# Kernel tuning notes

Hardware: AMD Instinct MI355X
Metric: run time of the kernel (lower is better)

The kernel has to match this reference:

```python
import jax, jax.numpy as jnp
import numpy as np

D_MODEL = 1024
NUM_HEAD = 16
D_K = D_MODEL // NUM_HEAD


def setup_inputs() -> dict:
    key = jax.random.key(0)
    ks = jax.random.split(key, 11)
    B, S = 2, 2048
    s = 1.0 / np.sqrt(D_MODEL)
    return {
        "q": jax.random.normal(ks[0], (B, S, D_MODEL), jnp.float32),
        "k": jax.random.normal(ks[1], (B, S, D_MODEL), jnp.float32),
        "v": jax.random.normal(ks[2], (B, S, D_MODEL), jnp.float32),
        "Wq": jax.random.normal(ks[3], (D_MODEL, D_MODEL), jnp.float32) * s,
        "bq": jnp.zeros((D_MODEL,), jnp.float32),
        "Wk": jax.random.normal(ks[4], (D_MODEL, D_MODEL), jnp.float32) * s,
        "bk": jnp.zeros((D_MODEL,), jnp.float32),
        "Wv": jax.random.normal(ks[5], (D_MODEL, D_MODEL), jnp.float32) * s,
        "bv": jnp.zeros((D_MODEL,), jnp.float32),
        "Wo": jax.random.normal(ks[6], (D_MODEL, D_MODEL), jnp.float32) * s,
        "bo": jnp.zeros((D_MODEL,), jnp.float32),
    }


def _split_head(x, B):
    # [B, S, d_model] -> [B, H, S, d_k]
    S = x.shape[1]
    return x.reshape(B, S, NUM_HEAD, D_K).transpose(0, 2, 1, 3)


def reference(q, k, v, Wq, bq, Wk, bk, Wv, bv, Wo, bo):
    B = q.shape[0]
    qh = _split_head(q @ Wq + bq, B)  # [B,H,Sq,dk]
    kh = _split_head(k @ Wk + bk, B)  # [B,H,Sk,dk]
    vh = _split_head(v @ Wv + bv, B)  # [B,H,Sk,dk]
    scores = jnp.einsum("bhqd,bhkd->bhqk", qh, kh) / jnp.sqrt(
        jnp.asarray(D_K, qh.dtype)
    )
    attn = jax.nn.softmax(scores, axis=-1)
    out = jnp.einsum("bhqk,bhkd->bhqd", attn, vh)  # [B,H,Sq,dk]
    out = out.transpose(0, 2, 1, 3).reshape(B, -1, D_MODEL)
    return jax.nn.relu(out @ Wo + bo)
```

## Files before the change

kernel.cpp:

```cpp
#include <hip/hip_runtime.h>
#include <math.h>

#define SEQ 2048
#define NHD 16

typedef float f32x4 __attribute__((ext_vector_type(4), may_alias));
typedef _Float16 h16x8 __attribute__((ext_vector_type(8), may_alias));
typedef _Float16 h16x4 __attribute__((ext_vector_type(4), may_alias));

__device__ __forceinline__ void gl_lds16(const void* g, void* l) {
  __builtin_amdgcn_global_load_lds(
      (const __attribute__((address_space(1))) unsigned int*)g,
      (__attribute__((address_space(3))) unsigned int*)l, 16, 0, 0);
}

struct PrepArgs {
  const float* W[4];
  _Float16* T[4];
  const float* X[3];
  _Float16* H[3];
};

__global__ __launch_bounds__(256) void prep_k(PrepArgs a) {
  __shared__ float tile[64][65];
  const int blk = blockIdx.x;
  const int t = threadIdx.x;
  if (blk < 1024) {
    const int widx = blk >> 8, tl = blk & 255;
    const int nb = (tl & 15) * 64, kb = (tl >> 4) * 64;
    const float* __restrict__ W = a.W[widx];
    _Float16* __restrict__ T = a.T[widx];
    const int c = t & 63, r0 = t >> 6;
#pragma unroll
    for (int i = 0; i < 16; ++i) {
      const int r = i * 4 + r0;
      tile[r][c] = W[(size_t)(kb + r) * 1024 + nb + c];
    }
    __syncthreads();
#pragma unroll
    for (int i = 0; i < 16; ++i) {
      const int n = i * 4 + r0;
      T[(size_t)(nb + n) * 1024 + kb + c] = (_Float16)tile[c][n];
    }
  } else {
    const int b2 = blk - 1024;
    const int z = b2 >> 11, bx = b2 & 2047;
    const float* __restrict__ X = a.X[z];
    _Float16* __restrict__ H = a.H[z];
    const size_t i = ((size_t)bx * 256 + t) * 8;
    const f32x4 f0 = *(const f32x4*)(X + i);
    const f32x4 f1 = *(const f32x4*)(X + i + 4);
    const float fs[8] = {f0.x, f0.y, f0.z, f0.w, f1.x, f1.y, f1.z, f1.w};
    h16x8 o;
#pragma unroll
    for (int j = 0; j < 8; ++j) o[j] = (_Float16)fs[j];
    *(h16x8*)(H + i) = o;
  }
}

struct QKVArgs {
  const _Float16* A[3];
  const _Float16* Bt[3];
  const float* bias[3];
  _Float16* C[3];
};

__global__ __launch_bounds__(512, 2) void gemm_qkv_k(QKVArgs a) {
  __shared__ __align__(16) char smem[131072];
  const int dblk = blockIdx.x;
  const int z = dblk >> 6;
  const int rb = dblk & 63;
  const int m0 = (rb >> 2) * 256;
  const int n0 = (rb & 3) * 256;
  const _Float16* __restrict__ A = a.A[z];
  const _Float16* __restrict__ Bt = a.Bt[z];
  const float* __restrict__ bias = a.bias[z];
  _Float16* __restrict__ C = a.C[z];

  const int t = threadIdx.x;
  const int l = t & 63, w = t >> 6;
  const int quad = l >> 4, l15 = l & 15;
  const int wm = w >> 2, wn = w & 3;

  const int srow = t >> 3;
  const int sslot = (t & 7) ^ (srow & 7);
  size_t goffA[4], goffB[4];
#pragma unroll
  for (int j = 0; j < 4; ++j) {
    goffA[j] = (size_t)(m0 + j * 64 + srow) * 1024 + sslot * 8;
    goffB[j] = (size_t)(n0 + j * 64 + srow) * 1024 + sslot * 8;
  }

  auto stage = [&](int buf, int kt) {
    const int k0 = kt * 64;
    char* base = smem + buf * 65536;
#pragma unroll
    for (int j = 0; j < 4; ++j) {
      gl_lds16(A + goffA[j] + k0, base + j * 8192 + w * 1024);
      gl_lds16(Bt + goffB[j] + k0, base + 32768 + j * 8192 + w * 1024);
    }
  };

  const f32x4 z4 = {0.f, 0.f, 0.f, 0.f};
  f32x4 acc[8][4];
#pragma unroll
  for (int i = 0; i < 8; ++i)
#pragma unroll
    for (int j = 0; j < 4; ++j) acc[i][j] = z4;

  const int xr = l15 & 7;

  stage(0, 0);
  for (int kt = 0; kt < 16; ++kt) {
    const int cur = kt & 1;
    if (kt < 15) {
      stage(cur ^ 1, kt + 1);
      asm volatile("s_waitcnt vmcnt(8)" ::: "memory");
    } else {
      asm volatile("s_waitcnt vmcnt(0)" ::: "memory");
    }
    __builtin_amdgcn_sched_barrier(0);
    __builtin_amdgcn_s_barrier();

    const char* base = smem + cur * 65536;
    h16x8 bf[4][2];
#pragma unroll
    for (int nj = 0; nj < 4; ++nj) {
      const int rowB = wn * 64 + nj * 16 + l15;
#pragma unroll
      for (int h = 0; h < 2; ++h) {
        const int sl = (h * 4 + quad) ^ xr;
        bf[nj][h] = *(const h16x8*)(base + 32768 + rowB * 128 + sl * 16);
      }
    }
#pragma unroll
    for (int mi = 0; mi < 8; ++mi) {
      const int rowA = wm * 128 + mi * 16 + l15;
      const h16x8 af0 = *(const h16x8*)(base + rowA * 128 + ((quad ^ xr) * 16));
      const h16x8 af1 = *(const h16x8*)(base + rowA * 128 + (((4 + quad) ^ xr) * 16));
#pragma unroll
      for (int nj = 0; nj < 4; ++nj) {
        acc[mi][nj] = __builtin_amdgcn_mfma_f32_16x16x32_f16(af0, bf[nj][0], acc[mi][nj], 0, 0, 0);
        acc[mi][nj] = __builtin_amdgcn_mfma_f32_16x16x32_f16(af1, bf[nj][1], acc[mi][nj], 0, 0, 0);
      }
    }
    __builtin_amdgcn_sched_barrier(0);
    __builtin_amdgcn_s_barrier();
  }

  if (z < 2) {
#pragma unroll
    for (int mi = 0; mi < 8; ++mi)
#pragma unroll
      for (int nj = 0; nj < 4; ++nj) {
        const int col = n0 + wn * 64 + nj * 16 + l15;
        const float bv = bias[col];
#pragma unroll
        for (int r = 0; r < 4; ++r) {
          const int row = m0 + wm * 128 + mi * 16 + quad * 4 + r;
          const int b = row >> 11, s = row & 2047;
          const int h = col >> 6, d = col & 63;
          C[((size_t)(b * NHD + h) * SEQ + s) * 64 + d] = (_Float16)(acc[mi][nj][r] + bv);
        }
      }
  } else {
    _Float16* sh = (_Float16*)smem;
#pragma unroll
    for (int mi = 0; mi < 8; ++mi)
#pragma unroll
      for (int nj = 0; nj < 4; ++nj) {
        const int col = wn * 64 + nj * 16 + l15;
        const float bv = bias[n0 + col];
#pragma unroll
        for (int r = 0; r < 4; ++r) {
          const int row = wm * 128 + mi * 16 + quad * 4 + r;
          sh[row * 256 + col] = (_Float16)(acc[mi][nj][r] + bv);
        }
      }
    __syncthreads();
    const int dr = t >> 1;
    const int half = t & 1;
    const int hh = dr >> 6, d = dr & 63;
    const int b = m0 >> 11, sbase = m0 & 2047;
    const int colL = hh * 64 + d;
    const size_t gbase =
        ((size_t)((b * NHD + (n0 >> 6) + hh) * 64 + d)) * SEQ + sbase + half * 128;
#pragma unroll
    for (int m8 = 0; m8 < 16; ++m8) {
      const int qq = half * 128 + m8 * 8;
      h16x8 ov;
#pragma unroll
      for (int j = 0; j < 8; ++j) {
        const int q = qq + j;
        const int g = q >> 6, p = q & 63;
        const int c = (((p >> 5) << 1) | ((p >> 2) & 1)) * 16 +
                      (((p >> 3) & 3) << 2) + (p & 3);
        ov[j] = sh[(g * 64 + c) * 256 + colL];
      }
      *(h16x8*)(C + gbase + m8 * 8) = ov;
    }
  }
}

__global__ __launch_bounds__(256) void gemm_o_k(
    const _Float16* __restrict__ Op0, const _Float16* __restrict__ Op1,
    const float* __restrict__ Lp, const _Float16* __restrict__ Bt,
    const float* __restrict__ bias, float* __restrict__ Cf) {
  __shared__ char smem[40960];
  float* inv_lds = (float*)(smem + 32768);
  const int rb = blockIdx.x;
  const int n0 = ((rb >> 3) & 7) * 128;
  const int m0 = ((((rb >> 6) << 3) | (rb & 7))) * 128;
  const int t = threadIdx.x;
  const int l = t & 63, w = t >> 6;
  const int quad = l >> 4, l15 = l & 15;
  const int wm = w >> 1, wn = w & 1;
  const int arow0 = t >> 2, aq = t & 3;

#pragma unroll
  for (int e = t; e < 2048; e += 256) {
    const int rl = e >> 4, hh = e & 15;
    const int m = m0 + rl;
    const int b = m >> 11, s = m & 2047;
    const size_t li = (size_t)(b * NHD + hh) * 2048 + s;
    inv_lds[e] = 1.f / (Lp[li] + Lp[65536 + li]);
  }
  __syncthreads();

  auto stageB = [&](int buf, int k0) {
#pragma unroll
    for (int it = 0; it < 2; ++it) {
      const int c = it * 4 + w;
      const int rr = c * 16 + l15;
      gl_lds16(Bt + (size_t)(n0 + rr) * 1024 + k0 + quad * 8,
               smem + buf * 8192 + c * 1024);
    }
  };
  auto loadA = [&](int k0, h16x8 (&r0)[2], h16x8 (&r1)[2]) {
#pragma unroll
    for (int it = 0; it < 2; ++it) {
      const size_t off = (size_t)(m0 + it * 64 + arow0) * 1024 + k0 + aq * 8;
      r0[it] = *(const h16x8*)(Op0 + off);
      r1[it] = *(const h16x8*)(Op1 + off);
    }
  };
  auto writeA = [&](int buf, int k0, const h16x8 (&r0)[2], const h16x8 (&r1)[2]) {
    const int head = k0 >> 6;
    h16x8* alds = (h16x8*)(smem + 16384 + buf * 8192);
#pragma unroll
    for (int it = 0; it < 2; ++it) {
      const int row = it * 64 + arow0;
      const int slot = (row >> 4) * 64 + aq * 16 + ((row & 15) ^ (aq * 2));
      const float inv = inv_lds[row * 16 + head];
      h16x8 hv;
#pragma unroll
      for (int j = 0; j < 8; ++j)
        hv[j] = (_Float16)(((float)r0[it][j] + (float)r1[it][j]) * inv);
      alds[slot] = hv;
    }
  };

  const f32x4 z4 = {0.f, 0.f, 0.f, 0.f};
  f32x4 acc[4][4];
#pragma unroll
  for (int i = 0; i < 4; ++i)
#pragma unroll
    for (int j = 0; j < 4; ++j) acc[i][j] = z4;

  h16x8 a0r[2], a1r[2];
  loadA(0, a0r, a1r);
  stageB(0, 0);
  writeA(0, 0, a0r, a1r);
  __syncthreads();
  int cur = 0;
  for (int k0 = 0; k0 < 1024; k0 += 32) {
    const int nk = k0 + 32;
    if (nk < 1024) {
      loadA(nk, a0r, a1r);
      stageB(cur ^ 1, nk);
    }
    const h16x8* blds = (const h16x8*)(smem + cur * 8192);
    const h16x8* alds = (const h16x8*)(smem + 16384 + cur * 8192);
    h16x8 af[4], bf[4];
#pragma unroll
    for (int i = 0; i < 4; ++i) {
      af[i] = alds[(wm * 4 + i) * 64 + quad * 16 + (l15 ^ (quad * 2))];
      bf[i] = blds[(wn * 4 + i) * 64 + l];
    }
#pragma unroll
    for (int i = 0; i < 4; ++i)
#pragma unroll
      for (int j = 0; j < 4; ++j)
        acc[i][j] = __builtin_amdgcn_mfma_f32_16x16x32_f16(af[i], bf[j], acc[i][j], 0, 0, 0);
    if (nk < 1024) writeA(cur ^ 1, nk, a0r, a1r);
    __syncthreads();
    cur ^= 1;
  }
#pragma unroll
  for (int i = 0; i < 4; ++i)
#pragma unroll
    for (int j = 0; j < 4; ++j) {
      const int col = n0 + wn * 64 + j * 16 + l15;
      const float bv = bias[col];
#pragma unroll
      for (int r = 0; r < 4; ++r) {
        const int row = m0 + wm * 64 + i * 16 + quad * 4 + r;
        Cf[(size_t)row * 1024 + col] = fmaxf(acc[i][j][r] + bv, 0.f);
      }
    }
}

__global__ __launch_bounds__(256, 4) void attn_k(
    const _Float16* __restrict__ Qf, const _Float16* __restrict__ Kf,
    const _Float16* __restrict__ Vtp,
    _Float16* __restrict__ Op0, _Float16* __restrict__ Op1,
    float* __restrict__ Lp) {
  __shared__ __align__(16) char smem[16384];
  h16x8* lds8 = (h16x8*)smem;
  const int dblk = blockIdx.x;
  const int comb = ((dblk >> 7) << 3) | (dblk & 7);
  const int q0 = ((dblk >> 3) & 15) * 128;
  const int bh = comb >> 1;
  const int kz = comb & 1;
  const int t = threadIdx.x;
  const int l = t & 63, w = t >> 6;
  const int quad = l >> 4, l15 = l & 15;
  const int b = bh >> 4, h = bh & 15;

  const _Float16* Kb = Kf + (size_t)bh * SEQ * 64;
  const _Float16* Vtb = Vtp + (size_t)bh * 64 * SEQ;

  h16x8 qf[2][2];
#pragma unroll
  for (int mi = 0; mi < 2; ++mi) {
    const size_t qb = ((size_t)bh * SEQ + q0 + w * 32 + mi * 16 + l15) * 64;
#pragma unroll
    for (int ks = 0; ks < 2; ++ks)
      qf[mi][ks] = *(const h16x8*)&Qf[qb + ks * 32 + quad * 8];
  }
  const _Float16 qs = (_Float16)0.125f;
#pragma unroll
  for (int mi = 0; mi < 2; ++mi)
#pragma unroll
    for (int ks = 0; ks < 2; ++ks) qf[mi][ks] = qf[mi][ks] * qs;

  const f32x4 z4 = {0.f, 0.f, 0.f, 0.f};
  f32x4 oacc[2][4];
  float lsum[2] = {0.f, 0.f};
#pragma unroll
  for (int mi = 0; mi < 2; ++mi)
#pragma unroll
    for (int i = 0; i < 4; ++i) oacc[mi][i] = z4;

  const int kbeg = kz * 1024;
  for (int k0 = kbeg; k0 < kbeg + 1024; k0 += 64) {
#pragma unroll
    for (int it = 0; it < 2; ++it) {
      const int c = it * 4 + w;
      const int kd = (c >> 1) * 16 + l15;
      const int off2 = (c & 1) * 32 + quad * 8;
      gl_lds16(Kb + (size_t)(k0 + kd) * 64 + off2, smem + c * 1024);
      gl_lds16(Vtb + (size_t)kd * SEQ + k0 + off2, smem + 8192 + c * 1024);
    }
    __syncthreads();

    h16x8 pa[2][2];
#pragma unroll
    for (int mi = 0; mi < 2; ++mi) {
      f32x4 sacc[4];
#pragma unroll
      for (int nt = 0; nt < 4; ++nt) {
        const h16x8 kf0 = lds8[(nt * 2 + 0) * 64 + l];
        const h16x8 kf1 = lds8[(nt * 2 + 1) * 64 + l];
        f32x4 s = z4;
        s = __builtin_amdgcn_mfma_f32_16x16x32_f16(kf0, qf[mi][0], s, 0, 0, 0);
        s = __builtin_amdgcn_mfma_f32_16x16x32_f16(kf1, qf[mi][1], s, 0, 0, 0);
        sacc[nt] = s;
      }
      float ls = 0.f;
#pragma unroll
      for (int r = 0; r < 4; ++r) {
        const _Float16 e0 = (_Float16)__expf(sacc[0][r]);
        const _Float16 e1 = (_Float16)__expf(sacc[1][r]);
        const _Float16 e2 = (_Float16)__expf(sacc[2][r]);
        const _Float16 e3 = (_Float16)__expf(sacc[3][r]);
        pa[mi][0][r] = e0;
        pa[mi][0][4 + r] = e1;
        pa[mi][1][r] = e2;
        pa[mi][1][4 + r] = e3;
        ls += (float)e0 + (float)e1 + (float)e2 + (float)e3;
      }
      lsum[mi] += ls;
    }

#pragma unroll
    for (int nt = 0; nt < 4; ++nt) {
      const h16x8 vf0 = lds8[512 + (nt * 2 + 0) * 64 + l];
      const h16x8 vf1 = lds8[512 + (nt * 2 + 1) * 64 + l];
#pragma unroll
      for (int mi = 0; mi < 2; ++mi) {
        oacc[mi][nt] = __builtin_amdgcn_mfma_f32_16x16x32_f16(pa[mi][0], vf0, oacc[mi][nt], 0, 0, 0);
        oacc[mi][nt] = __builtin_amdgcn_mfma_f32_16x16x32_f16(pa[mi][1], vf1, oacc[mi][nt], 0, 0, 0);
      }
    }
    __syncthreads();
  }

  _Float16* __restrict__ Op = kz ? Op1 : Op0;
#pragma unroll
  for (int mi = 0; mi < 2; ++mi)
#pragma unroll
    for (int nt = 0; nt < 4; ++nt)
#pragma unroll
      for (int r = 0; r < 4; ++r) {
        const size_t tok = (size_t)b * SEQ + q0 + w * 32 + mi * 16 + quad * 4 + r;
        Op[tok * 1024 + h * 64 + nt * 16 + l15] = (_Float16)oacc[mi][nt][r];
      }
#pragma unroll
  for (int mi = 0; mi < 2; ++mi) {
    float v = lsum[mi];
    v += __shfl_xor(v, 16);
    v += __shfl_xor(v, 32);
    if (quad == 0) {
      const int row = q0 + w * 32 + mi * 16 + l15;
      Lp[(size_t)kz * 65536 + bh * 2048 + row] = v;
    }
  }
}

extern "C" void kernel_launch(void* const* d_in, const int* in_sizes, int n_in,
                              void* d_out, int out_size, void* d_ws, size_t ws_size,
                              hipStream_t stream) {
  const float* q = (const float*)d_in[0];
  const float* k = (const float*)d_in[1];
  const float* v = (const float*)d_in[2];
  const float* Wq = (const float*)d_in[3];
  const float* bq = (const float*)d_in[4];
  const float* Wk = (const float*)d_in[5];
  const float* bk = (const float*)d_in[6];
  const float* Wv = (const float*)d_in[7];
  const float* bv = (const float*)d_in[8];
  const float* Wo = (const float*)d_in[9];
  const float* bo = (const float*)d_in[10];

  char* W8 = (char*)d_ws;
  const size_t MB = 1024 * 1024;
  auto F = [&](size_t off) { return (_Float16*)(W8 + off); };
  _Float16* wt[4] = {F(0), F(2 * MB), F(4 * MB), F(6 * MB)};
  _Float16* qf = F(8 * MB);
  _Float16* kf = F(16 * MB);
  _Float16* vf = F(24 * MB);
  _Float16* Qf = F(32 * MB);
  _Float16* Kf = F(40 * MB);
  _Float16* Vt = F(56 * MB);
  _Float16* Op0 = F(8 * MB);
  _Float16* Op1 = F(16 * MB);
  float* Lp = (float*)(W8 + 64 * MB);

  const dim3 blk(256);

  PrepArgs pa;
  pa.W[0] = Wq; pa.W[1] = Wk; pa.W[2] = Wv; pa.W[3] = Wo;
  pa.T[0] = wt[0]; pa.T[1] = wt[1]; pa.T[2] = wt[2]; pa.T[3] = wt[3];
  pa.X[0] = q; pa.X[1] = k; pa.X[2] = v;
  pa.H[0] = qf; pa.H[1] = kf; pa.H[2] = vf;
  prep_k<<<dim3(7168), blk, 0, stream>>>(pa);

  QKVArgs qa;
  qa.A[0] = qf; qa.A[1] = kf; qa.A[2] = vf;
  qa.Bt[0] = wt[0]; qa.Bt[1] = wt[1]; qa.Bt[2] = wt[2];
  qa.bias[0] = bq; qa.bias[1] = bk; qa.bias[2] = bv;
  qa.C[0] = Qf; qa.C[1] = Kf; qa.C[2] = Vt;
  gemm_qkv_k<<<dim3(192), dim3(512), 0, stream>>>(qa);

  attn_k<<<dim3(1024), blk, 0, stream>>>(Qf, Kf, Vt, Op0, Op1, Lp);
  gemm_o_k<<<dim3(256), blk, 0, stream>>>(Op0, Op1, Lp, wt[3], bo, (float*)d_out);
}
```

Baseline: 232.9 us.

## Halve attention query tile to 64 rows and double grid for occupancy

Each attention block now processes 64 query rows instead of 128, with each wave handling one 16-row MFMA tile rather than two. The grid doubles to 2048 blocks and launch bounds raise the target to 8 blocks per SM, aiming for more resident waves to hide latency. In exchange each K/V tile loaded into LDS is reused by half as many queries, doubling K/V global and LDS traffic per unit of work.

New measurement: 256.6 us. 1.1x slower.

```diff
diff --git a/kernel.cpp b/kernel.cpp
--- a/kernel.cpp
+++ b/kernel.cpp
@@ -310,7 +310,7 @@
     }
 }
 
-__global__ __launch_bounds__(256, 4) void attn_k(
+__global__ __launch_bounds__(256, 8) void attn_k(
     const _Float16* __restrict__ Qf, const _Float16* __restrict__ Kf,
     const _Float16* __restrict__ Vtp,
     _Float16* __restrict__ Op0, _Float16* __restrict__ Op1,
@@ -318,8 +318,8 @@
   __shared__ __align__(16) char smem[16384];
   h16x8* lds8 = (h16x8*)smem;
   const int dblk = blockIdx.x;
-  const int comb = ((dblk >> 7) << 3) | (dblk & 7);
-  const int q0 = ((dblk >> 3) & 15) * 128;
+  const int comb = ((dblk >> 8) << 3) | (dblk & 7);
+  const int q0 = ((dblk >> 3) & 31) * 64;
   const int bh = comb >> 1;
   const int kz = comb & 1;
   const int t = threadIdx.x;
@@ -330,27 +330,21 @@
   const _Float16* Kb = Kf + (size_t)bh * SEQ * 64;
   const _Float16* Vtb = Vtp + (size_t)bh * 64 * SEQ;
 
-  h16x8 qf[2][2];
-#pragma unroll
-  for (int mi = 0; mi < 2; ++mi) {
-    const size_t qb = ((size_t)bh * SEQ + q0 + w * 32 + mi * 16 + l15) * 64;
-#pragma unroll
-    for (int ks = 0; ks < 2; ++ks)
-      qf[mi][ks] = *(const h16x8*)&Qf[qb + ks * 32 + quad * 8];
-  }
-  const _Float16 qs = (_Float16)0.125f;
-#pragma unroll
-  for (int mi = 0; mi < 2; ++mi)
-#pragma unroll
-    for (int ks = 0; ks < 2; ++ks) qf[mi][ks] = qf[mi][ks] * qs;
+  h16x8 qf[2];
+  {
+    const size_t qb = ((size_t)bh * SEQ + q0 + w * 16 + l15) * 64;
+    qf[0] = *(const h16x8*)&Qf[qb + quad * 8];
+    qf[1] = *(const h16x8*)&Qf[qb + 32 + quad * 8];
+    const _Float16 qs = (_Float16)0.125f;
+    qf[0] = qf[0] * qs;
+    qf[1] = qf[1] * qs;
+  }
 
   const f32x4 z4 = {0.f, 0.f, 0.f, 0.f};
-  f32x4 oacc[2][4];
-  float lsum[2] = {0.f, 0.f};
-#pragma unroll
-  for (int mi = 0; mi < 2; ++mi)
-#pragma unroll
-    for (int i = 0; i < 4; ++i) oacc[mi][i] = z4;
+  f32x4 oacc[4];
+  float lsum = 0.f;
+#pragma unroll
+  for (int i = 0; i < 4; ++i) oacc[i] = z4;
 
   const int kbeg = kz * 1024;
   for (int k0 = kbeg; k0 < kbeg + 1024; k0 += 64) {
@@ -364,65 +358,49 @@
     }
     __syncthreads();
 
-    h16x8 pa[2][2];
-#pragma unroll
-    for (int mi = 0; mi < 2; ++mi) {
-      f32x4 sacc[4];
-#pragma unroll
-      for (int nt = 0; nt < 4; ++nt) {
-        const h16x8 kf0 = lds8[(nt * 2 + 0) * 64 + l];
-        const h16x8 kf1 = lds8[(nt * 2 + 1) * 64 + l];
-        f32x4 s = z4;
-        s = __builtin_amdgcn_mfma_f32_16x16x32_f16(kf0, qf[mi][0], s, 0, 0, 0);
-        s = __builtin_amdgcn_mfma_f32_16x16x32_f16(kf1, qf[mi][1], s, 0, 0, 0);
-        sacc[nt] = s;
-      }
-      float ls = 0.f;
+    h16x8 pa0, pa1;
+#pragma unroll
+    for (int nt = 0; nt < 4; ++nt) {
+      const h16x8 kf0 = lds8[(nt * 2 + 0) * 64 + l];
+      const h16x8 kf1 = lds8[(nt * 2 + 1) * 64 + l];
+      f32x4 s = z4;
+      s = __builtin_amdgcn_mfma_f32_16x16x32_f16(kf0, qf[0], s, 0, 0, 0);
+      s = __builtin_amdgcn_mfma_f32_16x16x32_f16(kf1, qf[1], s, 0, 0, 0);
 #pragma unroll
       for (int r = 0; r < 4; ++r) {
-        const _Float16 e0 = (_Float16)__expf(sacc[0][r]);
-        const _Float16 e1 = (_Float16)__expf(sacc[1][r]);
-        const _Float16 e2 = (_Float16)__expf(sacc[2][r]);
-        const _Float16 e3 = (_Float16)__expf(sacc[3][r]);
-        pa[mi][0][r] = e0;
-        pa[mi][0][4 + r] = e1;
-        pa[mi][1][r] = e2;
-        pa[mi][1][4 + r] = e3;
-        ls += (float)e0 + (float)e1 + (float)e2 + (float)e3;
-      }
-      lsum[mi] += ls;
+        const _Float16 e = (_Float16)__expf(s[r]);
+        if (nt == 0) pa0[r] = e;
+        else if (nt == 1) pa0[4 + r] = e;
+        else if (nt == 2) pa1[r] = e;
+        else pa1[4 + r] = e;
+        lsum += (float)e;
+      }
     }
 
 #pragma unroll
     for (int nt = 0; nt < 4; ++nt) {
       const h16x8 vf0 = lds8[512 + (nt * 2 + 0) * 64 + l];
       const h16x8 vf1 = lds8[512 + (nt * 2 + 1) * 64 + l];
-#pragma unroll
-      for (int mi = 0; mi < 2; ++mi) {
-        oacc[mi][nt] = __builtin_amdgcn_mfma_f32_16x16x32_f16(pa[mi][0], vf0, oacc[mi][nt], 0, 0, 0);
-        oacc[mi][nt] = __builtin_amdgcn_mfma_f32_16x16x32_f16(pa[mi][1], vf1, oacc[mi][nt], 0, 0, 0);
-      }
+      oacc[nt] = __builtin_amdgcn_mfma_f32_16x16x32_f16(pa0, vf0, oacc[nt], 0, 0, 0);
+      oacc[nt] = __builtin_amdgcn_mfma_f32_16x16x32_f16(pa1, vf1, oacc[nt], 0, 0, 0);
     }
     __syncthreads();
   }
 
   _Float16* __restrict__ Op = kz ? Op1 : Op0;
 #pragma unroll
-  for (int mi = 0; mi < 2; ++mi)
-#pragma unroll
-    for (int nt = 0; nt < 4; ++nt)
-#pragma unroll
-      for (int r = 0; r < 4; ++r) {
-        const size_t tok = (size_t)b * SEQ + q0 + w * 32 + mi * 16 + quad * 4 + r;
-        Op[tok * 1024 + h * 64 + nt * 16 + l15] = (_Float16)oacc[mi][nt][r];
-      }
-#pragma unroll
-  for (int mi = 0; mi < 2; ++mi) {
-    float v = lsum[mi];
+  for (int nt = 0; nt < 4; ++nt)
+#pragma unroll
+    for (int r = 0; r < 4; ++r) {
+      const size_t tok = (size_t)b * SEQ + q0 + w * 16 + quad * 4 + r;
+      Op[tok * 1024 + h * 64 + nt * 16 + l15] = (_Float16)oacc[nt][r];
+    }
+  {
+    float v = lsum;
     v += __shfl_xor(v, 16);
     v += __shfl_xor(v, 32);
     if (quad == 0) {
-      const int row = q0 + w * 32 + mi * 16 + l15;
+      const int row = q0 + w * 16 + l15;
       Lp[(size_t)kz * 65536 + bh * 2048 + row] = v;
     }
   }
@@ -473,6 +451,6 @@
   qa.C[0] = Qf; qa.C[1] = Kf; qa.C[2] = Vt;
   gemm_qkv_k<<<dim3(192), dim3(512), 0, stream>>>(qa);
 
-  attn_k<<<dim3(1024), blk, 0, stream>>>(Qf, Kf, Vt, Op0, Op1, Lp);
+  attn_k<<<dim3(2048), blk, 0, stream>>>(Qf, Kf, Vt, Op0, Op1, Lp);
   gemm_o_k<<<dim3(256), blk, 0, stream>>>(Op0, Op1, Lp, wt[3], bo, (float*)d_out);
 }
```
